# Kernel optimization log

Measured on AMD Instinct MI355X. Metric: run time of the kernel, lower is better.

Reference implementation:

```python
import jax, jax.numpy as jnp
import numpy as np

B, T, D_FEAT, FREQ, HID = 256, 128, 128, 16, 128


def setup_inputs() -> dict:
    key = jax.random.key(0)
    ks = jax.random.split(key, 14)
    n = lambda k, s, sc: jax.random.normal(k, s, jnp.float32) * sc
    sx = float(np.sqrt(2.0 / (D_FEAT + HID)))   # xavier-ish for W_*
    sf = float(np.sqrt(2.0 / (D_FEAT + FREQ)))
    sh = float(np.sqrt(1.0 / HID))              # stand-in for orthogonal U_*
    return {
        "input": jax.random.normal(ks[0], (B, D_FEAT * T), jnp.float32),
        "W_i": n(ks[1], (D_FEAT, HID), sx), "U_i": n(ks[2], (HID, HID), sh), "b_i": jnp.zeros((HID,), jnp.float32),
        "W_ste": n(ks[3], (D_FEAT, HID), sx), "U_ste": n(ks[4], (HID, HID), sh), "b_ste": jnp.ones((HID,), jnp.float32),
        "W_fre": n(ks[5], (D_FEAT, FREQ), sf), "U_fre": n(ks[6], (HID, FREQ), sh), "b_fre": jnp.ones((FREQ,), jnp.float32),
        "W_c": n(ks[7], (D_FEAT, HID), sx), "U_c": n(ks[8], (HID, HID), sh), "b_c": jnp.zeros((HID,), jnp.float32),
        "W_o": n(ks[9], (D_FEAT, HID), sx), "U_o": n(ks[10], (HID, HID), sh), "b_o": jnp.zeros((HID,), jnp.float32),
        "U_a": n(ks[11], (FREQ, 1), sh), "b_a": jnp.zeros((HID,), jnp.float32),
        "W_sym": n(ks[12], (HID, 1), sh), "b_sym": jnp.zeros((1,), jnp.float32),
    }


def _hsig(z):  # torch.nn.Hardsigmoid: relu6(x+3)/6
    return jnp.clip(z / 6.0 + 0.5, 0.0, 1.0)


def reference(input, W_i, U_i, b_i, W_ste, U_ste, b_ste, W_fre, U_fre, b_fre,
              W_c, U_c, b_c, W_o, U_o, b_o, U_a, b_a, W_sym, b_sym):
    Bsz = input.shape[0]
    x = input.reshape(Bsz, D_FEAT, -1).transpose(0, 2, 1)  # (B, T, D)
    # hoist the 5 input projections out of the time loop (identical math)
    xi = jnp.einsum('btd,dh->tbh', x, W_i) + b_i
    xste = jnp.einsum('btd,dh->tbh', x, W_ste) + b_ste
    xfre = jnp.einsum('btd,df->tbf', x, W_fre) + b_fre
    xc = jnp.einsum('btd,dh->tbh', x, W_c) + b_c
    xo = jnp.einsum('btd,dh->tbh', x, W_o) + b_o
    frequency = jnp.arange(FREQ, dtype=jnp.float32) / FREQ
    two_pi = jnp.float32(2.0 * np.pi)
    ua = U_a[:, 0]  # (FREQ,)

    def step(carry, xs):
        h, S_re, S_im, t = carry
        xi_t, xste_t, xfre_t, xc_t, xo_t = xs
        i = _hsig(xi_t + h @ U_i)
        ste = _hsig(xste_t + h @ U_ste)
        fre = _hsig(xfre_t + h @ U_fre)
        f = ste[:, :, None] * fre[:, None, :]          # (B, H, F)
        c = i * jnp.tanh(xc_t + h @ U_c)               # (B, H)
        t = t + 1.0
        omega = two_pi * t * frequency                 # (F,)
        S_re = f * S_re + c[:, :, None] * jnp.cos(omega)
        S_im = f * S_im + c[:, :, None] * jnp.sin(omega)
        A = S_re * S_re + S_im * S_im                  # (B, H, F)
        a = jnp.tanh(jnp.einsum('bhf,f->bh', A, ua) + b_a)
        o = _hsig(xo_t + h @ U_o)
        h = o * a
        return (h, S_re, S_im, t), None

    init = (jnp.zeros((Bsz, HID), jnp.float32),
            jnp.zeros((Bsz, HID, FREQ), jnp.float32),
            jnp.zeros((Bsz, HID, FREQ), jnp.float32),
            jnp.float32(0.0))
    (h, _, _, _), _ = jax.lax.scan(step, init, (xi, xste, xfre, xc, xo))
    return h @ W_sym + b_sym  # (B, num_symbols)
```

## Files before the change

kernel.cpp:

```cpp
#include <hip/hip_runtime.h>
#include <hip/hip_bf16.h>


__device__ __forceinline__ float hsig_f(float z) {
    return fminf(fmaxf(z * (1.0f / 6.0f) + 0.5f, 0.0f), 1.0f);
}

__global__ __launch_bounds__(256) void proj_gemm(
    const float* __restrict__ input,
    const float* __restrict__ Wi, const float* __restrict__ Wste,
    const float* __restrict__ Wc, const float* __restrict__ Wo,
    const float* __restrict__ Wfre,
    const float* __restrict__ bi, const float* __restrict__ bste,
    const float* __restrict__ bc, const float* __restrict__ bo,
    const float* __restrict__ bfre,
    float* __restrict__ P)
{
    __shared__ __align__(16) float XT[128 * 64];
    __shared__ __align__(16) float WT[128 * 66];

    const int br  = blockIdx.x;
    const int b   = br >> 1;
    const int t0g = (br & 1) * 64;
    const int tid = threadIdx.x;

    const float* xb = input + (size_t)b * 16384 + t0g;
#pragma unroll
    for (int i = 0; i < 8; i++) {
        int f = (i * 256 + tid) * 4;
        int k = f >> 6, t = f & 63;
        *(float4*)(&XT[k * 64 + t]) = *(const float4*)(xb + k * 128 + t);
    }

    const int tx = tid & 31;
    const int ty = tid >> 5;

    const float* Ws[5]     = {Wi, Wste, Wc, Wo, Wfre};
    const float* biases[5] = {bi, bste, bc, bo, bfre};

    for (int ct = 0; ct < 5; ct++) {
        const float* W     = Ws[ct];
        const float* bias  = biases[ct];
        const int    ncols = (ct < 4) ? 128 : 16;
        const int    npass = (ct < 4) ? 2 : 1;
        const int    cbase = (ct < 4) ? ct * 128 : 512;

        for (int ch = 0; ch < npass; ch++) {
            __syncthreads();
#pragma unroll
            for (int i = 0; i < 8; i++) {
                int f = (i * 256 + tid) * 4;
                int k = f >> 6, c = f & 63;
                int gc = ch * 64 + c;
                if (gc < ncols)
                    *(float4*)(&WT[k * 66 + c]) = *(const float4*)(W + k * ncols + gc);
            }
            __syncthreads();

            float acc[8][2] = {};
#pragma unroll 4
            for (int k = 0; k < 128; k++) {
                float2 w  = *(const float2*)(&WT[k * 66 + tx * 2]);
                float4 x0 = *(const float4*)(&XT[k * 64 + ty * 8]);
                float4 x1 = *(const float4*)(&XT[k * 64 + ty * 8 + 4]);
                const float xr[8] = {x0.x, x0.y, x0.z, x0.w, x1.x, x1.y, x1.z, x1.w};
#pragma unroll
                for (int r = 0; r < 8; r++) {
                    acc[r][0] = fmaf(xr[r], w.x, acc[r][0]);
                    acc[r][1] = fmaf(xr[r], w.y, acc[r][1]);
                }
            }

            const int colg = ch * 64 + tx * 2;
            if (colg < ncols) {
                float b0 = bias[colg], b1 = bias[colg + 1];
#pragma unroll
                for (int r = 0; r < 8; r++) {
                    int row = br * 64 + ty * 8 + r;
                    float2 o = make_float2(acc[r][0] + b0, acc[r][1] + b1);
                    *(float2*)(&P[(size_t)row * 528 + cbase + colg]) = o;
                }
            }
        }
    }
}

__global__
__attribute__((amdgpu_flat_work_group_size(1024, 1024)))
__attribute__((amdgpu_waves_per_eu(4, 4)))
void recur_kernel(
    const float* __restrict__ P,
    const float* __restrict__ Ui, const float* __restrict__ Uste,
    const float* __restrict__ Uc, const float* __restrict__ Uo,
    const float* __restrict__ Ufre,
    const float* __restrict__ Ua, const float* __restrict__ ba_g,
    const float* __restrict__ Wsym, const float* __restrict__ bsym,
    float* __restrict__ out)
{
    __shared__ float ufre_t[16 * 132];
    __shared__ float costab[16], sintab[16];
    __shared__ float gate_buf[512];
    __shared__ float partial_buf[512];
    __shared__ float fre_buf[16];
    __shared__ float h_buf[128];

    const int tid  = threadIdx.x;
    const int lane = tid & 63;
    const int half = tid >> 9;
    const int c    = tid & 511;
    const int m    = c >> 7;
    const int j    = c & 127;
    const int hh   = tid >> 3;
    const int fsel = tid & 7;
    const int b    = blockIdx.x;

    for (int e = tid; e < 2048; e += 1024) {
        int k = e >> 4, col = e & 15;
        ufre_t[col * 132 + k] = Ufre[e];
    }
    if (tid < 16) {
        float ang = 6.283185307179586f * (float)tid * (1.0f / 16.0f);
        costab[tid] = cosf(ang);
        sintab[tid] = sinf(ang);
    }
    if (tid < 128) h_buf[tid] = 0.0f;

    const float* Uptr = (m == 0) ? Ui : (m == 1) ? Uste : (m == 2) ? Uc : Uo;
    const volatile float* Uv = (const volatile float*)Uptr;
    float Ucol[64];
#pragma unroll
    for (int k = 0; k < 64; k++) Ucol[k] = Uv[(half * 64 + k) * 128 + j];
    asm volatile("" ::: "memory");

    const float ua0 = Ua[fsel];
    const float ua1 = Ua[fsel + 8];
    const float ba  = ba_g[hh];

    float hA = 0.0f;
    float Sre0 = 0.f, Sim0 = 0.f, Sre1 = 0.f, Sim1 = 0.f;
    int idx0 = 0, idx1 = 0;

    __syncthreads();

    const float* pr = P + (size_t)b * 128 * 528;
    for (int t = 0; t < 128; t++) {
        const float xpre = (half == 0) ? pr[c] : pr[512 + (c >> 5)];

        float a0 = 0.f, a1 = 0.f;
#pragma unroll
        for (int kk = 0; kk < 64; kk += 2) {
            float s0 = __uint_as_float(__builtin_amdgcn_readlane(__float_as_uint(hA), kk));
            float s1 = __uint_as_float(__builtin_amdgcn_readlane(__float_as_uint(hA), kk + 1));
            a0 = fmaf(s0, Ucol[kk],     a0);
            a1 = fmaf(s1, Ucol[kk + 1], a1);
        }
        float acc = a0 + a1;

        if (half) partial_buf[c] = acc;
        __syncthreads();

        if (half == 0) {
            float z = acc + partial_buf[c] + xpre;
            float g = (m == 2) ? tanhf(z) : hsig_f(z);
            gate_buf[c] = g;
        } else {
            const int col = c >> 5, kg = c & 31;
            float4 hv = *(const float4*)(&h_buf[kg * 4]);
            float4 uv = *(const float4*)(&ufre_t[col * 132 + kg * 4]);
            float p = fmaf(hv.x, uv.x, fmaf(hv.y, uv.y, fmaf(hv.z, uv.z, hv.w * uv.w)));
#pragma unroll
            for (int off = 1; off <= 16; off <<= 1) p += __shfl_xor(p, off, 64);
            if (kg == 0) fre_buf[col] = hsig_f(p + xpre);
        }
        __syncthreads();

        {
            float iv = gate_buf[hh];
            float sv = gate_buf[128 + hh];
            float tc = gate_buf[256 + hh];
            float ov = gate_buf[384 + hh];
            float cg = iv * tc;

            idx0 = (idx0 + fsel) & 15;
            idx1 = (idx1 + fsel + 8) & 15;

            float f0v = sv * fre_buf[fsel];
            float f1v = sv * fre_buf[fsel + 8];
            Sre0 = fmaf(f0v, Sre0, cg * costab[idx0]);
            Sim0 = fmaf(f0v, Sim0, cg * sintab[idx0]);
            Sre1 = fmaf(f1v, Sre1, cg * costab[idx1]);
            Sim1 = fmaf(f1v, Sim1, cg * sintab[idx1]);

            float aacc = fmaf(Sre0, Sre0, Sim0 * Sim0) * ua0;
            aacc = fmaf(fmaf(Sre1, Sre1, Sim1 * Sim1), ua1, aacc);
            aacc += __shfl_xor(aacc, 1, 64);
            aacc += __shfl_xor(aacc, 2, 64);
            aacc += __shfl_xor(aacc, 4, 64);
            if (fsel == 0) {
                float a = tanhf(aacc + ba);
                h_buf[hh] = ov * a;
            }
        }
        __syncthreads();
        hA = h_buf[half * 64 + lane];
        pr += 528;
    }

    if (tid < 64) {
        float v = fmaf(h_buf[lane], Wsym[lane], h_buf[64 + lane] * Wsym[64 + lane]);
#pragma unroll
        for (int off = 1; off <= 32; off <<= 1) v += __shfl_xor(v, off, 64);
        if (lane == 0) out[b] = v + bsym[0];
    }
}

extern "C" void kernel_launch(void* const* d_in, const int* in_sizes, int n_in,
                              void* d_out, int out_size, void* d_ws, size_t ws_size,
                              hipStream_t stream) {
    const float* input = (const float*)d_in[0];
    const float* W_i   = (const float*)d_in[1];
    const float* U_i   = (const float*)d_in[2];
    const float* b_i   = (const float*)d_in[3];
    const float* W_ste = (const float*)d_in[4];
    const float* U_ste = (const float*)d_in[5];
    const float* b_ste = (const float*)d_in[6];
    const float* W_fre = (const float*)d_in[7];
    const float* U_fre = (const float*)d_in[8];
    const float* b_fre = (const float*)d_in[9];
    const float* W_c   = (const float*)d_in[10];
    const float* U_c   = (const float*)d_in[11];
    const float* b_c   = (const float*)d_in[12];
    const float* W_o   = (const float*)d_in[13];
    const float* U_o   = (const float*)d_in[14];
    const float* b_o   = (const float*)d_in[15];
    const float* U_a   = (const float*)d_in[16];
    const float* b_a   = (const float*)d_in[17];
    const float* W_sym = (const float*)d_in[18];
    const float* b_sym = (const float*)d_in[19];

    float* P = (float*)d_ws;

    proj_gemm<<<512, 256, 0, stream>>>(
        input, W_i, W_ste, W_c, W_o, W_fre,
        b_i, b_ste, b_c, b_o, b_fre, P);

    recur_kernel<<<256, 1024, 0, stream>>>(
        P, U_i, U_ste, U_c, U_o, U_fre,
        U_a, b_a, W_sym, b_sym, (float*)d_out);
}
```

Before: 412.4 us.

## Store recurrent U weights as fp16 pairs in LDS instead of registers

Moves the four 128x128 recurrent weight matrices out of per-thread registers (64 floats each) into shared memory, packed as half2 pairs, and reads them from LDS every timestep. It also drops the explicit waves-per-eu attribute in favour of plain launch bounds. The aim is to relieve register pressure and the spilling that comes with it. The cost is an LDS read on every step of the recurrence, lower weight precision that can compound over 128 steps, and 128KB of LDS per block, which limits occupancy to one block per CU.

```diff
diff --git a/kernel.cpp b/kernel.cpp
--- a/kernel.cpp
+++ b/kernel.cpp
@@ -1,5 +1,6 @@
 #include <hip/hip_runtime.h>
 #include <hip/hip_bf16.h>
+#include <hip/hip_fp16.h>
 
 
 __device__ __forceinline__ float hsig_f(float z) {
@@ -85,10 +86,7 @@
     }
 }
 
-__global__
-__attribute__((amdgpu_flat_work_group_size(1024, 1024)))
-__attribute__((amdgpu_waves_per_eu(4, 4)))
-void recur_kernel(
+__global__ __launch_bounds__(1024) void recur_kernel(
     const float* __restrict__ P,
     const float* __restrict__ Ui, const float* __restrict__ Uste,
     const float* __restrict__ Uc, const float* __restrict__ Uo,
@@ -97,6 +95,7 @@
     const float* __restrict__ Wsym, const float* __restrict__ bsym,
     float* __restrict__ out)
 {
+    __shared__ __half2 u16_lds[4 * 64 * 128];
     __shared__ float ufre_t[16 * 132];
     __shared__ float costab[16], sintab[16];
     __shared__ float gate_buf[512];
@@ -114,6 +113,13 @@
     const int fsel = tid & 7;
     const int b    = blockIdx.x;
 
+    for (int e = tid; e < 4 * 64 * 128; e += 1024) {
+        int m_ = e >> 13, rem = e & 8191, kk = rem >> 7, jj = rem & 127;
+        const float* Um = (m_ == 0) ? Ui : (m_ == 1) ? Uste : (m_ == 2) ? Uc : Uo;
+        float lo = Um[(2 * kk) * 128 + jj];
+        float hi = Um[(2 * kk + 1) * 128 + jj];
+        u16_lds[e] = __floats2half2_rn(lo, hi);
+    }
     for (int e = tid; e < 2048; e += 1024) {
         int k = e >> 4, col = e & 15;
         ufre_t[col * 132 + k] = Ufre[e];
@@ -125,13 +131,6 @@
     }
     if (tid < 128) h_buf[tid] = 0.0f;
 
-    const float* Uptr = (m == 0) ? Ui : (m == 1) ? Uste : (m == 2) ? Uc : Uo;
-    const volatile float* Uv = (const volatile float*)Uptr;
-    float Ucol[64];
-#pragma unroll
-    for (int k = 0; k < 64; k++) Ucol[k] = Uv[(half * 64 + k) * 128 + j];
-    asm volatile("" ::: "memory");
-
     const float ua0 = Ua[fsel];
     const float ua1 = Ua[fsel + 8];
     const float ba  = ba_g[hh];
@@ -142,17 +141,20 @@
 
     __syncthreads();
 
+    const __half2* ucol = &u16_lds[(m << 13) + (half << 12) + j];
+
     const float* pr = P + (size_t)b * 128 * 528;
     for (int t = 0; t < 128; t++) {
         const float xpre = (half == 0) ? pr[c] : pr[512 + (c >> 5)];
 
         float a0 = 0.f, a1 = 0.f;
 #pragma unroll
-        for (int kk = 0; kk < 64; kk += 2) {
-            float s0 = __uint_as_float(__builtin_amdgcn_readlane(__float_as_uint(hA), kk));
-            float s1 = __uint_as_float(__builtin_amdgcn_readlane(__float_as_uint(hA), kk + 1));
-            a0 = fmaf(s0, Ucol[kk],     a0);
-            a1 = fmaf(s1, Ucol[kk + 1], a1);
+        for (int kk = 0; kk < 32; kk++) {
+            __half2 uh = ucol[kk << 7];
+            float s0 = __uint_as_float(__builtin_amdgcn_readlane(__float_as_uint(hA), 2 * kk));
+            float s1 = __uint_as_float(__builtin_amdgcn_readlane(__float_as_uint(hA), 2 * kk + 1));
+            a0 = fmaf(__low2float(uh),  s0, a0);
+            a1 = fmaf(__high2float(uh), s1, a1);
         }
         float acc = a0 + a1;
 
```

Result: slower. 429.5 us (+4.1%).
